# Performance work log

Hardware: AMD Instinct MI355X
Metric: run time of the kernel (lower is better)

The kernel has to match this reference:

```python
import jax, jax.numpy as jnp
import numpy as np

N_PTS = 262144      # 512x512 coordinate grid
N_HEADS = 16
HID = 256
N_HID_LAYERS = 3
IN_F = 2
OUT_F = 3
PE_L = 10                  # NeRF positional-encoding frequencies
PE_DIM = 2 * IN_F * PE_L   # sin+cos per freq per coord = 40
CAP = N_PTS // N_HEADS     # balanced partition: points per head


def positional_encoding(x):
    # x: [..., IN_F] -> [..., PE_DIM]
    freqs = (2.0 ** jnp.arange(PE_L, dtype=x.dtype)) * jnp.pi          # [L]
    ang = x[..., None, :] * freqs[:, None]                              # [..., L, IN_F]
    pe = jnp.concatenate([jnp.sin(ang), jnp.cos(ang)], axis=-1)        # [..., L, 2*IN_F]
    return pe.reshape(*x.shape[:-1], PE_DIM)


def setup_inputs() -> dict:
    key = jax.random.key(0)
    ks = jax.random.split(key, 5)
    # Balanced random segment map (equivalent to the module's segment_weight),
    # converted to the static routing table the torch loop recomputes each step:
    # head_idx[h] = where(segment_weight == h)
    rng = np.random.default_rng(0)
    seg = rng.permutation(np.arange(N_PTS) % N_HEADS)
    head_idx = np.stack([np.where(seg == h)[0] for h in range(N_HEADS)]).astype(np.int32)  # [H, CAP]

    coords = jax.random.uniform(ks[0], (1, N_PTS, IN_F), minval=-1.0, maxval=1.0)

    def he(k, shape, fan_in):
        return jax.random.normal(k, shape, dtype=jnp.float32) * np.float32(np.sqrt(2.0 / fan_in))

    W_in = he(ks[1], (N_HEADS, PE_DIM, HID), PE_DIM)
    b_in = jnp.zeros((N_HEADS, HID), jnp.float32)
    W_hid = he(ks[2], (N_HEADS, N_HID_LAYERS, HID, HID), HID)
    b_hid = jnp.zeros((N_HEADS, N_HID_LAYERS, HID), jnp.float32)
    W_out = he(ks[3], (N_HEADS, HID, OUT_F), HID)
    b_out = jnp.zeros((N_HEADS, OUT_F), jnp.float32)

    return dict(coords=coords, head_idx=jnp.asarray(head_idx),
                W_in=W_in, b_in=b_in, W_hid=W_hid, b_hid=b_hid,
                W_out=W_out, b_out=b_out)


def reference(coords, head_idx, W_in, b_in, W_hid, b_hid, W_out, b_out):
    # --- dispatch: gather each head's points (torch: coords[:, index, :]) ---
    coords_h = coords[0][head_idx]                                      # [H, CAP, IN_F]
    # --- per-head MLP (relu_MLP with positional embedding) ---
    h = jax.nn.relu(jnp.einsum('hcd,hdf->hcf', positional_encoding(coords_h), W_in)
                    + b_in[:, None, :])                                 # [H, CAP, HID]
    for l in range(N_HID_LAYERS):
        h = jax.nn.relu(jnp.einsum('hcf,hfg->hcg', h, W_hid[:, l])
                        + b_hid[:, l, None, :])
    out_h = jnp.einsum('hcf,hfo->hco', h, W_out) + b_out[:, None, :]    # [H, CAP, OUT_F]
    # --- combine: scatter per-head outputs back (torch: output_final[0, index, :] = out) ---
    out_final = jnp.zeros((1, N_PTS, OUT_F), coords.dtype)
    out_final = out_final.at[0, head_idx.reshape(-1)].set(out_h.reshape(-1, OUT_F))
    return (out_final, coords)
```

## Files before the change

kernel.cpp:

```cpp
#include <hip/hip_runtime.h>

typedef unsigned short u16;
typedef unsigned int   u32;
typedef __bf16  bf16x8 __attribute__((ext_vector_type(8)));
typedef float   f32x16 __attribute__((ext_vector_type(16)));

#define CAP      16384
#define L0_ELS   (256*56)
#define HID_ELS  (256*256)
#define OUT_ELS  (32*256)
#define HEAD_WS  (L0_ELS + 3*HID_ELS + OUT_ELS)
#define HID_OFF  L0_ELS
#define OUT_OFF  (L0_ELS + 3*HID_ELS)

union F8 { u32 u[4]; bf16x8 v; };

__device__ __forceinline__ u16 f2b(float f) {
  u32 u = __float_as_uint(f); u += 0x7fffu + ((u >> 16) & 1u); return (u16)(u >> 16);
}
__device__ __forceinline__ u32 packbf2(float a, float b) {
  u32 ua = __float_as_uint(a); ua += 0x7fffu + ((ua >> 16) & 1u);
  u32 ub = __float_as_uint(b); ub += 0x7fffu + ((ub >> 16) & 1u);
  return (ua >> 16) | (ub & 0xffff0000u);
}

__device__ __forceinline__ f32x16 mfma16(bf16x8 a, bf16x8 b, f32x16 c) {
  return __builtin_amdgcn_mfma_f32_32x32x16_bf16(a, b, c, 0, 0, 0);
}

__device__ __forceinline__ void stage_async(const u16* __restrict__ g, short* l,
                                            int bytes, int tid) {
  for (int base = tid * 16; base < bytes; base += 4096)
    __builtin_amdgcn_global_load_lds(
        (const __attribute__((address_space(1))) u32*)((const char*)g + base),
        (__attribute__((address_space(3))) u32*)((char*)l + base), 16, 0, 0);
}

__device__ __forceinline__ bf16x8 fragL0(const short* sl, int i, int t, int n, int hh) {
  return *(const bf16x8*)((const char*)sl + (32*i + n)*112 + (2*t + hh)*16);
}
__device__ __forceinline__ bf16x8 fragH(const short* sl, int i, int t, int n, int hh) {
  return *(const bf16x8*)((const char*)sl + ((32*i + n) << 9) + (((2*t + hh) ^ (n & 7)) << 4));
}

__device__ __forceinline__ void load_bias_raw(const float* b, int r, int hh, float4 o[4]) {
#pragma unroll
  for (int g = 0; g < 4; ++g) o[g] = *(const float4*)(b + 32*r + 8*g + 4*hh);
}
__device__ __forceinline__ f32x16 bias_to_acc(const float4 raw[4]) {
  f32x16 a;
#pragma unroll
  for (int g = 0; g < 4; ++g) {
    a[4*g+0] = raw[g].x; a[4*g+1] = raw[g].y;
    a[4*g+2] = raw[g].z; a[4*g+3] = raw[g].w;
  }
  return a;
}

__device__ __forceinline__ void epilogue(f32x16 c, int hh, F8& t0, F8& t1) {
  u32 P[8];
#pragma unroll
  for (int i = 0; i < 8; ++i)
    P[i] = packbf2(fmaxf(c[2*i], 0.f), fmaxf(c[2*i+1], 0.f));
  u32 s0 = hh ? P[0] : P[2], s1 = hh ? P[1] : P[3];
  u32 s2 = hh ? P[4] : P[6], s3 = hh ? P[5] : P[7];
  u32 x0 = __shfl_xor(s0, 32, 64), x1 = __shfl_xor(s1, 32, 64);
  u32 x2 = __shfl_xor(s2, 32, 64), x3 = __shfl_xor(s3, 32, 64);
  t0.u[0] = hh ? x0 : P[0]; t0.u[1] = hh ? x1 : P[1];
  t0.u[2] = hh ? P[2] : x0; t0.u[3] = hh ? P[3] : x1;
  t1.u[0] = hh ? x2 : P[4]; t1.u[1] = hh ? x3 : P[5];
  t1.u[2] = hh ? P[6] : x2; t1.u[3] = hh ? P[7] : x3;
}

__global__ void prep(const float* __restrict__ W_in, const float* __restrict__ b_in,
                     const float* __restrict__ W_hid, const float* __restrict__ W_out,
                     u16* __restrict__ ws) {
  const int ct = blockIdx.x * 256 + threadIdx.x;
  const int head = ct / 27392;
  const int r = ct - head * 27392;
  u16 v[8]; int dst;
  if (r < 1792) {
    const int nn = r / 7, k0 = (r % 7) * 8;
#pragma unroll
    for (int j = 0; j < 8; ++j) {
      const int k = k0 + j;
      v[j] = (k < 40) ? f2b(W_in[head*10240 + k*256 + nn])
           : (k == 40) ? f2b(b_in[head*256 + nn]) : (u16)0;
    }
    dst = head*HEAD_WS + nn*56 + k0;
  } else if (r < 26368) {
    const int q = r - 1792, l = q >> 13, q2 = q & 8191;
    const int nn = q2 >> 5, cc = q2 & 31, kb = 8 * (cc ^ (nn & 7));
#pragma unroll
    for (int j = 0; j < 8; ++j)
      v[j] = f2b(W_hid[head*196608 + l*65536 + (kb + j)*256 + nn]);
    dst = head*HEAD_WS + HID_OFF + l*65536 + nn*256 + cc*8;
  } else {
    const int q = r - 26368;
    const int nn = q >> 5, cc = q & 31, kb = 8 * (cc ^ (nn & 7));
#pragma unroll
    for (int j = 0; j < 8; ++j)
      v[j] = (nn < 3) ? f2b(W_out[head*768 + (kb + j)*3 + nn]) : (u16)0;
    dst = head*HEAD_WS + OUT_OFF + nn*256 + cc*8;
  }
  uint4 o;
  o.x = (u32)v[0] | ((u32)v[1] << 16); o.y = (u32)v[2] | ((u32)v[3] << 16);
  o.z = (u32)v[4] | ((u32)v[5] << 16); o.w = (u32)v[6] | ((u32)v[7] << 16);
  *(uint4*)(ws + dst) = o;
}

__global__ void copy_coords(const uint4* __restrict__ s, uint4* __restrict__ d) {
  const int i = blockIdx.x * 256 + threadIdx.x;
  d[i] = s[i];
}

__launch_bounds__(256, 2)
__global__ void mlp_main(const float* __restrict__ coords, const int* __restrict__ head_idx,
                         const float* __restrict__ b_hid, const float* __restrict__ b_out,
                         const u16* __restrict__ ws, float* __restrict__ out) {
  __shared__ short ring[2 * 16384];
  const int tid = threadIdx.x;
  const int lane = tid & 63, wv = tid >> 6;
  const int n = lane & 31, hh = lane >> 5;
  const int head = blockIdx.x & 15, chunk = blockIdx.x >> 4;
  const u16* wsh = ws + head * HEAD_WS;

  stage_async(wsh + 0*3584, ring,          7168, tid);
  stage_async(wsh + 1*3584, ring + 16384,  7168, tid);

  const int pt = chunk*128 + wv*32 + n;
  const int g  = head_idx[head*CAP + pt];
  const float2 cxy = *(const float2*)(coords + 2*g);
  const float xs = cxy.x, ys = cxy.y;
  const float bo0 = b_out[head*3+0], bo1 = b_out[head*3+1], bo2 = b_out[head*3+2];

  F8 pe[3];
#pragma unroll
  for (int t = 0; t < 3; ++t) {
    float e[8];
#pragma unroll
    for (int half = 0; half < 2; ++half) {
      const int l = 4*t + 2*hh + half;
      if (l < 10) {
        const float fr = 3.14159265358979323846f * (float)(1 << l);
        float s1, c1, s2, c2;
        sincosf(xs * fr, &s1, &c1);
        sincosf(ys * fr, &s2, &c2);
        e[4*half+0] = s1; e[4*half+1] = s2; e[4*half+2] = c1; e[4*half+3] = c2;
      } else {
        e[4*half+0] = (l == 10) ? 1.0f : 0.0f;
        e[4*half+1] = 0.f; e[4*half+2] = 0.f; e[4*half+3] = 0.f;
      }
    }
    pe[t].u[0] = packbf2(e[0], e[1]); pe[t].u[1] = packbf2(e[2], e[3]);
    pe[t].u[2] = packbf2(e[4], e[5]); pe[t].u[3] = packbf2(e[6], e[7]);
  }

  F8 act0[16], act1[16];
  __syncthreads();

#pragma unroll
  for (int rp = 0; rp < 4; ++rp) {
    short* sl = ring + (rp & 1) * 16384;
    f32x16 acc0 = (f32x16)0.f, acc1 = (f32x16)0.f;
#pragma unroll
    for (int t = 0; t < 3; ++t) {
      acc0 = mfma16(fragL0(sl, 0, t, n, hh), pe[t].v, acc0);
      acc1 = mfma16(fragL0(sl, 1, t, n, hh), pe[t].v, acc1);
    }
    __syncthreads();
    const u16* src = (rp < 2) ? (wsh + (rp + 2)*3584) : (wsh + HID_OFF + (rp - 2)*16384);
    const int bytes = (rp < 2) ? 7168 : 32768;
    stage_async(src, sl, bytes, tid);
    epilogue(acc0, hh, act0[4*rp+0], act0[4*rp+1]);
    epilogue(acc1, hh, act0[4*rp+2], act0[4*rp+3]);
  }

  auto hid_layer = [&](const float* bias, F8 (&ain)[16], F8 (&aout)[16],
                       const u16* j0, const u16* j1, const u16* j2, const u16* j3,
                       int b2, int b3) {
    float4 bc0[4], bc1[4], bn0[4], bn1[4];
    load_bias_raw(bias, 0, hh, bc0); load_bias_raw(bias, 1, hh, bc1);
    const u16* jsrc[4] = { j0, j1, j2, j3 };
    const int  jb[4]   = { 32768, 32768, b2, b3 };
#pragma unroll
    for (int rp = 0; rp < 4; ++rp) {
      short* sl = ring + (rp & 1) * 16384;
      if (rp < 3) { load_bias_raw(bias, 2*rp+2, hh, bn0); load_bias_raw(bias, 2*rp+3, hh, bn1); }
      f32x16 acc0 = bias_to_acc(bc0);
      f32x16 acc1 = bias_to_acc(bc1);
#pragma unroll
      for (int t = 0; t < 16; ++t) {
        bf16x8 a0 = fragH(sl, 0, t, n, hh);
        bf16x8 a1 = fragH(sl, 1, t, n, hh);
        acc0 = mfma16(a0, ain[t].v, acc0);
        acc1 = mfma16(a1, ain[t].v, acc1);
      }
      __syncthreads();
      if (jb[rp] > 0) stage_async(jsrc[rp], sl, jb[rp], tid);
      epilogue(acc0, hh, aout[4*rp+0], aout[4*rp+1]);
      epilogue(acc1, hh, aout[4*rp+2], aout[4*rp+3]);
      if (rp < 3) {
#pragma unroll
        for (int q = 0; q < 4; ++q) { bc0[q] = bn0[q]; bc1[q] = bn1[q]; }
      }
    }
  };

  const u16* hb = wsh + HID_OFF;
  hid_layer(b_hid + (head*3+0)*256, act0, act1,
            hb + 2*16384, hb + 3*16384, hb + HID_ELS, hb + HID_ELS + 16384, 32768, 32768);
  hid_layer(b_hid + (head*3+1)*256, act1, act0,
            hb + HID_ELS + 2*16384, hb + HID_ELS + 3*16384,
            hb + 2*HID_ELS, hb + 2*HID_ELS + 16384, 32768, 32768);
  hid_layer(b_hid + (head*3+2)*256, act0, act1,
            hb + 2*HID_ELS + 2*16384, hb + 2*HID_ELS + 3*16384,
            wsh + OUT_OFF, (const u16*)0, 16384, 0);

  f32x16 acc = (f32x16)0.f;
#pragma unroll
  for (int t = 0; t < 16; ++t)
    acc = mfma16(fragH(ring, 0, t, n, hh), act1[t].v, acc);
  if (hh == 0) {
    const long base = (long)g * 3;
    out[base + 0] = acc[0] + bo0;
    out[base + 1] = acc[1] + bo1;
    out[base + 2] = acc[2] + bo2;
  }
}

extern "C" void kernel_launch(void* const* d_in, const int* in_sizes, int n_in,
                              void* d_out, int out_size, void* d_ws, size_t ws_size,
                              hipStream_t stream) {
  const float* coords   = (const float*)d_in[0];
  const int*   head_idx = (const int*)d_in[1];
  const float* W_in     = (const float*)d_in[2];
  const float* b_in     = (const float*)d_in[3];
  const float* W_hid    = (const float*)d_in[4];
  const float* b_hid    = (const float*)d_in[5];
  const float* W_out    = (const float*)d_in[6];
  const float* b_out    = (const float*)d_in[7];
  float* out = (float*)d_out;
  u16*   ws  = (u16*)d_ws;
  if (ws_size < (size_t)HEAD_WS * 16 * sizeof(u16)) return;

  prep<<<dim3(1712), dim3(256), 0, stream>>>(W_in, b_in, W_hid, W_out, ws);
  copy_coords<<<dim3(512), dim3(256), 0, stream>>>((const uint4*)coords, (uint4*)(out + 786432));
  mlp_main<<<dim3(2048), dim3(256), 0, stream>>>(coords, head_idx, b_hid, b_out, ws, out);
}
```

Before: 220.1 us.

## Permute hidden-weight K order to drop cross-lane shuffles in epilogue

The MFMA accumulator-to-operand epilogue previously needed four cross-half-wave shuffles per tile to rebuild the bf16 operand fragments. The weight prep kernel now permutes the K dimension of hidden and output weights with a fixed sigma mapping, so each lane's accumulator values can be packed directly into the next layer's B fragment with no shuffle. This removes DPP/permute traffic and select instructions from every epilogue. Correctness depends on the permutation exactly matching the accumulator register layout.

After: 309.5 us. 1.41x slower.

```diff
diff --git a/kernel.cpp b/kernel.cpp
--- a/kernel.cpp
+++ b/kernel.cpp
@@ -57,19 +57,18 @@
   return a;
 }
 
-__device__ __forceinline__ void epilogue(f32x16 c, int hh, F8& t0, F8& t1) {
-  u32 P[8];
-#pragma unroll
-  for (int i = 0; i < 8; ++i)
-    P[i] = packbf2(fmaxf(c[2*i], 0.f), fmaxf(c[2*i+1], 0.f));
-  u32 s0 = hh ? P[0] : P[2], s1 = hh ? P[1] : P[3];
-  u32 s2 = hh ? P[4] : P[6], s3 = hh ? P[5] : P[7];
-  u32 x0 = __shfl_xor(s0, 32, 64), x1 = __shfl_xor(s1, 32, 64);
-  u32 x2 = __shfl_xor(s2, 32, 64), x3 = __shfl_xor(s3, 32, 64);
-  t0.u[0] = hh ? x0 : P[0]; t0.u[1] = hh ? x1 : P[1];
-  t0.u[2] = hh ? P[2] : x0; t0.u[3] = hh ? P[3] : x1;
-  t1.u[0] = hh ? x2 : P[4]; t1.u[1] = hh ? x3 : P[5];
-  t1.u[2] = hh ? P[6] : x2; t1.u[3] = hh ? P[7] : x3;
+__device__ __forceinline__ void epilogue(f32x16 c, F8& t0, F8& t1) {
+#pragma unroll
+  for (int g = 0; g < 4; ++g) {
+    t0.u[g] = packbf2(fmaxf(c[2*g],   0.f), fmaxf(c[2*g+1],   0.f));
+    t1.u[g] = packbf2(fmaxf(c[8+2*g], 0.f), fmaxf(c[8+2*g+1], 0.f));
+  }
+}
+
+__device__ __forceinline__ int sigma_k(int k) {
+  const int hh  = (k >> 3) & 1;
+  const int reg = (k & 7) + 8 * ((k >> 4) & 1);
+  return (k & ~31) + (reg & 3) + 8 * (reg >> 2) + 4 * hh;
 }
 
 __global__ void prep(const float* __restrict__ W_in, const float* __restrict__ b_in,
@@ -93,14 +92,14 @@
     const int nn = q2 >> 5, cc = q2 & 31, kb = 8 * (cc ^ (nn & 7));
 #pragma unroll
     for (int j = 0; j < 8; ++j)
-      v[j] = f2b(W_hid[head*196608 + l*65536 + (kb + j)*256 + nn]);
+      v[j] = f2b(W_hid[head*196608 + l*65536 + sigma_k(kb + j)*256 + nn]);
     dst = head*HEAD_WS + HID_OFF + l*65536 + nn*256 + cc*8;
   } else {
     const int q = r - 26368;
     const int nn = q >> 5, cc = q & 31, kb = 8 * (cc ^ (nn & 7));
 #pragma unroll
     for (int j = 0; j < 8; ++j)
-      v[j] = (nn < 3) ? f2b(W_out[head*768 + (kb + j)*3 + nn]) : (u16)0;
+      v[j] = (nn < 3) ? f2b(W_out[head*768 + sigma_k(kb + j)*3 + nn]) : (u16)0;
     dst = head*HEAD_WS + OUT_OFF + nn*256 + cc*8;
   }
   uint4 o;
@@ -172,8 +171,8 @@
     const u16* src = (rp < 2) ? (wsh + (rp + 2)*3584) : (wsh + HID_OFF + (rp - 2)*16384);
     const int bytes = (rp < 2) ? 7168 : 32768;
     stage_async(src, sl, bytes, tid);
-    epilogue(acc0, hh, act0[4*rp+0], act0[4*rp+1]);
-    epilogue(acc1, hh, act0[4*rp+2], act0[4*rp+3]);
+    epilogue(acc0, act0[4*rp+0], act0[4*rp+1]);
+    epilogue(acc1, act0[4*rp+2], act0[4*rp+3]);
   }
 
   auto hid_layer = [&](const float* bias, F8 (&ain)[16], F8 (&aout)[16],
@@ -198,8 +197,8 @@
       }
       __syncthreads();
       if (jb[rp] > 0) stage_async(jsrc[rp], sl, jb[rp], tid);
-      epilogue(acc0, hh, aout[4*rp+0], aout[4*rp+1]);
-      epilogue(acc1, hh, aout[4*rp+2], aout[4*rp+3]);
+      epilogue(acc0, aout[4*rp+0], aout[4*rp+1]);
+      epilogue(acc1, aout[4*rp+2], aout[4*rp+3]);
       if (rp < 3) {
 #pragma unroll
         for (int q = 0; q < 4; ++q) { bc0[q] = bn0[q]; bc1[q] = bn1[q]; }
```
